# Kernel tuning notes

Hardware: AMD Instinct MI355X
Metric: run time of the kernel (lower is better)

The kernel has to match this reference:

```python
import jax, jax.numpy as jnp
import numpy as np

DMODEL = 1024
Q_HEADS = 16
KV_HEADS = 4
DHEAD = 64
SEQ = 2048
TOP_K = 64
ROPE_BASE = 10000.0
NEG_INF = -1e30  # stand-in for -inf that is safe under softmax


def rope_cos_sin(seq_len, dhead, base):
    inv_freq = 1.0 / (base ** (jnp.arange(0, dhead, 2, dtype=jnp.float32) / dhead))  # [dhead/2]
    t = jnp.arange(seq_len, dtype=jnp.float32)
    angles = jnp.outer(t, inv_freq)                       # [S, dhead/2]
    emb = jnp.concatenate([angles, angles], axis=-1)      # [S, dhead]
    return jnp.cos(emb), jnp.sin(emb)


def rotate_half(x):
    x1, x2 = jnp.split(x, 2, axis=-1)
    return jnp.concatenate([-x2, x1], axis=-1)


def apply_rope(x, cos, sin):
    # x: [B, H, S, dhead]; cos/sin: [S, dhead]
    return x * cos[None, None] + rotate_half(x) * sin[None, None]


def setup_inputs() -> dict:
    key = jax.random.key(0)
    ks = jax.random.split(key, 5)
    s = 0.02
    return {
        "x": jax.random.normal(ks[0], (1, SEQ, DMODEL), jnp.float32),
        "Wq": jax.random.normal(ks[1], (Q_HEADS * DHEAD, DMODEL), jnp.float32) * s,
        "Wk": jax.random.normal(ks[2], (KV_HEADS * DHEAD, DMODEL), jnp.float32) * s,
        "Wv": jax.random.normal(ks[3], (KV_HEADS * DHEAD, DMODEL), jnp.float32) * s,
        "Wo": jax.random.normal(ks[4], (DMODEL, Q_HEADS * DHEAD), jnp.float32) * s,
    }


def reference(x, Wq, Wk, Wv, Wo):
    B, S, _ = x.shape
    cos, sin = rope_cos_sin(S, DHEAD, ROPE_BASE)

    q = (x @ Wq.T).reshape(B, S, Q_HEADS, DHEAD).transpose(0, 2, 1, 3)   # [B,Hq,S,d]
    k = (x @ Wk.T).reshape(B, S, KV_HEADS, DHEAD).transpose(0, 2, 1, 3)  # [B,Hkv,S,d]
    v = (x @ Wv.T).reshape(B, S, KV_HEADS, DHEAD).transpose(0, 2, 1, 3)

    q = apply_rope(q, cos, sin)
    k = apply_rope(k, cos, sin)

    groups = Q_HEADS // KV_HEADS  # repeat_kv
    k = jnp.repeat(k, groups, axis=1)  # [B,Hq,S,d]
    v = jnp.repeat(v, groups, axis=1)

    scores = jnp.einsum("bhqd,bhkd->bhqk", q, k) / np.sqrt(DHEAD)  # [B,H,S,S]

    causal_mask = jnp.triu(jnp.ones((S, S), bool), k=1)
    scores = jnp.where(causal_mask[None, None], NEG_INF, scores)

    # top-k mask before softmax
    topk_vals, _ = jax.lax.top_k(scores, TOP_K)            # [B,H,S,K]
    threshold = topk_vals[..., -1:]                         # kth largest
    scores = jnp.where(scores < threshold, NEG_INF, scores)

    weights = jax.nn.softmax(scores, axis=-1)
    out = jnp.einsum("bhqk,bhkd->bhqd", weights, v)         # [B,H,S,d]
    out = out.transpose(0, 2, 1, 3).reshape(B, S, Q_HEADS * DHEAD)
    return out @ Wo.T
```

## Files before the change

### kernel.cpp

```cpp
#include <hip/hip_runtime.h>
#include <hip/hip_bf16.h>
#include <math.h>

#define SEQ 2048
#define DMODEL 1024
#define QH 16
#define KVH 4
#define DH 64
#define TOPK 64
#define KV_D (KVH * DH)
#define CCAP 512
#define SROW 1028

typedef __attribute__((ext_vector_type(8))) short short8;
typedef __attribute__((ext_vector_type(4))) float floatx4;

__device__ __forceinline__ unsigned f2u(float f) {
    unsigned u = __float_as_uint(f);
    return (u & 0x80000000u) ? ~u : (u | 0x80000000u);
}
__device__ __forceinline__ float u2f(unsigned u) {
    unsigned v = (u & 0x80000000u) ? (u & 0x7fffffffu) : ~u;
    return __uint_as_float(v);
}
__device__ __forceinline__ unsigned short f2bf(float x) {
    unsigned u = __float_as_uint(x);
    return (unsigned short)((u + 0x7fffu + ((u >> 16) & 1u)) >> 16);
}
__device__ __forceinline__ float bf2f(unsigned short h) {
    return __uint_as_float((unsigned)h << 16);
}
__device__ __forceinline__ void split4(float4 f, ushort4& h, ushort4& l) {
    h.x = f2bf(f.x); l.x = f2bf(f.x - bf2f(h.x));
    h.y = f2bf(f.y); l.y = f2bf(f.y - bf2f(h.y));
    h.z = f2bf(f.z); l.z = f2bf(f.z - bf2f(h.z));
    h.w = f2bf(f.w); l.w = f2bf(f.w - bf2f(h.w));
}

__global__ __launch_bounds__(256) void cvt_all(const float* __restrict__ x,
                                               const float* __restrict__ Wq,
                                               const float* __restrict__ Wk,
                                               const float* __restrict__ Wv,
                                               const float* __restrict__ Wo,
                                               unsigned short* __restrict__ xhi,
                                               unsigned short* __restrict__ xlo,
                                               unsigned short* __restrict__ wbhi,
                                               unsigned short* __restrict__ wblo,
                                               unsigned short* __restrict__ wo,
                                               float* __restrict__ cosT,
                                               float* __restrict__ sinT) {
    int idx = blockIdx.x * 256 + threadIdx.x;
    if (idx >= 1196032) return;
    float4 f;
    ushort4 h, l;
    if (idx < 524288) {
        f = ((const float4*)x)[idx];
        split4(f, h, l);
        ((ushort4*)xhi)[idx] = h;
        ((ushort4*)xlo)[idx] = l;
    } else if (idx < 786432) {
        int s = idx - 524288;
        f = ((const float4*)Wq)[s];
        split4(f, h, l);
        ((ushort4*)wbhi)[s] = h;
        ((ushort4*)wblo)[s] = l;
    } else if (idx < 851968) {
        int s = idx - 786432;
        f = ((const float4*)Wk)[s];
        split4(f, h, l);
        ((ushort4*)wbhi)[idx - 524288] = h;
        ((ushort4*)wblo)[idx - 524288] = l;
    } else if (idx < 917504) {
        int s = idx - 851968;
        f = ((const float4*)Wv)[s];
        split4(f, h, l);
        ((ushort4*)wbhi)[idx - 524288] = h;
        ((ushort4*)wblo)[idx - 524288] = l;
    } else if (idx < 1179648) {
        int s = idx - 917504;
        f = ((const float4*)Wo)[s];
        ushort4 o;
        o.x = f2bf(f.x); o.y = f2bf(f.y); o.z = f2bf(f.z); o.w = f2bf(f.w);
        ((ushort4*)wo)[s] = o;
    } else {
        int s = idx - 1179648;
        int e0 = s * 4;
        float ft = (float)(e0 >> 5);
        int d0 = e0 & 31;
        float4 cw, sw;
#pragma unroll
        for (int k = 0; k < 4; ++k) {
            float inv = powf(10000.0f, -(float)(d0 + k) * (1.0f / 32.0f));
            float ss, cc;
            sincosf(ft * inv, &ss, &cc);
            ((float*)&cw)[k] = cc;
            ((float*)&sw)[k] = ss;
        }
        ((float4*)cosT)[s] = cw;
        ((float4*)sinT)[s] = sw;
    }
}

__device__ __forceinline__ void async16(const void* g, void* l) {
    __builtin_amdgcn_global_load_lds(
        (const __attribute__((address_space(1))) unsigned int*)g,
        (__attribute__((address_space(3))) unsigned int*)l, 16, 0, 0);
}

__global__ __launch_bounds__(256, 2) void gemm_qkv(const unsigned short* __restrict__ Ah,
                                                   const unsigned short* __restrict__ Al,
                                                   const unsigned short* __restrict__ Bh,
                                                   const unsigned short* __restrict__ Bl,
                                                   const float* __restrict__ cosT,
                                                   const float* __restrict__ sinT,
                                                   unsigned short* __restrict__ qhi,
                                                   unsigned short* __restrict__ qlo,
                                                   unsigned short* __restrict__ khi,
                                                   unsigned short* __restrict__ klo,
                                                   float* __restrict__ vv) {
    const int K = DMODEL;
    __shared__ unsigned short lAh[128 * 32];
    __shared__ unsigned short lAl[128 * 32];
    __shared__ unsigned short lBh[128 * 32];
    __shared__ unsigned short lBl[128 * 32];
    const int tid = threadIdx.x;
    const int lane = tid & 63;
    const int wid = tid >> 6;
    const int m0 = blockIdx.y * 128, n0 = blockIdx.x * 128;
    const int mq = (wid >> 1) * 64, nq = (wid & 1) * 64;
    const bool isv = (n0 >= 1280);

    floatx4 acc[4][4];
#pragma unroll
    for (int a = 0; a < 4; ++a)
#pragma unroll
        for (int b = 0; b < 4; ++b) acc[a][b] = (floatx4){0.f, 0.f, 0.f, 0.f};

    const int srow = tid >> 2;
    const int skb = (tid & 3) ^ ((tid >> 3) & 3);
    const size_t goff = (size_t)srow * K + skb * 8;
    const size_t goff2 = goff + (size_t)64 * K;
    const unsigned short* pAh = Ah + (size_t)m0 * K;
    const unsigned short* pAl = Al + (size_t)m0 * K;
    const unsigned short* pBh = Bh + (size_t)n0 * K;
    const unsigned short* pBl = Bl + (size_t)n0 * K;
    unsigned lbase = __builtin_amdgcn_readfirstlane((unsigned)(wid * 1024));

    for (int k0 = 0; k0 < K; k0 += 32) {
        async16(pAh + goff + k0, (char*)lAh + lbase);
        async16(pAh + goff2 + k0, (char*)lAh + lbase + 4096);
        async16(pBh + goff + k0, (char*)lBh + lbase);
        async16(pBh + goff2 + k0, (char*)lBh + lbase + 4096);
        if (!isv) {
            async16(pAl + goff + k0, (char*)lAl + lbase);
            async16(pAl + goff2 + k0, (char*)lAl + lbase + 4096);
            async16(pBl + goff + k0, (char*)lBl + lbase);
            async16(pBl + goff2 + k0, (char*)lBl + lbase + 4096);
        }
        __syncthreads();

        short8 ah[4], al[4], bh[4], bl[4];
#pragma unroll
        for (int mt = 0; mt < 4; ++mt) {
            int row = mq + mt * 16 + (lane & 15);
            int s = ((lane >> 4) ^ ((row >> 1) & 3)) * 8;
            ah[mt] = *(const short8*)&lAh[row * 32 + s];
            if (!isv) al[mt] = *(const short8*)&lAl[row * 32 + s];
        }
#pragma unroll
        for (int nt = 0; nt < 4; ++nt) {
            int row = nq + nt * 16 + (lane & 15);
            int s = ((lane >> 4) ^ ((row >> 1) & 3)) * 8;
            bh[nt] = *(const short8*)&lBh[row * 32 + s];
            if (!isv) bl[nt] = *(const short8*)&lBl[row * 32 + s];
        }
        if (isv) {
#pragma unroll
            for (int mt = 0; mt < 4; ++mt)
#pragma unroll
                for (int nt = 0; nt < 4; ++nt)
                    acc[mt][nt] = __builtin_amdgcn_mfma_f32_16x16x32_bf16(ah[mt], bh[nt], acc[mt][nt], 0, 0, 0);
        } else {
#pragma unroll
            for (int mt = 0; mt < 4; ++mt)
#pragma unroll
                for (int nt = 0; nt < 4; ++nt) {
                    floatx4 a = acc[mt][nt];
                    a = __builtin_amdgcn_mfma_f32_16x16x32_bf16(al[mt], bh[nt], a, 0, 0, 0);
                    a = __builtin_amdgcn_mfma_f32_16x16x32_bf16(ah[mt], bl[nt], a, 0, 0, 0);
                    a = __builtin_amdgcn_mfma_f32_16x16x32_bf16(ah[mt], bh[nt], a, 0, 0, 0);
                    acc[mt][nt] = a;
                }
        }
        __syncthreads();
    }

    if (!isv) {
        const bool isq = (n0 < 1024);
        const float qsc = isq ? 0.125f : 1.0f;
#pragma unroll
        for (int mt = 0; mt < 4; ++mt)
#pragma unroll
            for (int nt = 0; nt < 2; ++nt) {
                const int d32 = nt * 16 + (lane & 15);
#pragma unroll
                for (int rr = 0; rr < 4; ++rr) {
                    int row = m0 + mq + mt * 16 + (lane >> 4) * 4 + rr;
                    float lo = acc[mt][nt][rr], hi = acc[mt][nt + 2][rr];
                    float c = cosT[row * 32 + d32], s = sinT[row * 32 + d32];
                    float rlo = (lo * c - hi * s) * qsc;
                    float rhi = (hi * c + lo * s) * qsc;
                    unsigned short hlo = f2bf(rlo), hhi = f2bf(rhi);
                    unsigned short llo = f2bf(rlo - bf2f(hlo));
                    unsigned short lhi = f2bf(rhi - bf2f(hhi));
                    if (isq) {
                        size_t o = (size_t)row * DMODEL + n0 + nq + d32;
                        qhi[o] = hlo; qhi[o + 32] = hhi;
                        qlo[o] = llo; qlo[o + 32] = lhi;
                    } else {
                        int kvh = (n0 + nq - 1024) >> 6;
                        size_t o = ((size_t)kvh * SEQ + row) * DH + d32;
                        khi[o] = hlo; khi[o + 32] = hhi;
                        klo[o] = llo; klo[o + 32] = lhi;
                    }
                }
            }
    } else {
#pragma unroll
        for (int mt = 0; mt < 4; ++mt)
#pragma unroll
            for (int nt = 0; nt < 4; ++nt) {
                int vcol = n0 + nq + nt * 16 + (lane & 15) - 1280;
                int rbase = m0 + mq + mt * 16 + (lane >> 4) * 4;
#pragma unroll
                for (int rr = 0; rr < 4; ++rr)
                    vv[(size_t)(rbase + rr) * KV_D + vcol] = acc[mt][nt][rr];
            }
    }
}

__global__ __launch_bounds__(256, 2) void gemm_wo(const unsigned short* __restrict__ A,
                                                  const unsigned short* __restrict__ B,
                                                  float* __restrict__ C) {
    const int N = DMODEL, K = DMODEL;
    __shared__ unsigned short lAs[64 * 32];
    __shared__ unsigned short lBs[128 * 32];
    const int tid = threadIdx.x;
    const int lane = tid & 63;
    const int wid = tid >> 6;
    const int m0 = blockIdx.y * 64, n0 = blockIdx.x * 128;

    floatx4 acc[4][2];
#pragma unroll
    for (int a = 0; a < 4; ++a)
#pragma unroll
        for (int b = 0; b < 2; ++b) acc[a][b] = (floatx4){0.f, 0.f, 0.f, 0.f};

    const int srow = tid >> 2;
    const int skb = (tid & 3) ^ ((tid >> 3) & 3);
    const unsigned short* Ag = A + (size_t)(m0 + srow) * K + skb * 8;
    const unsigned short* Bg = B + (size_t)(n0 + srow) * K + skb * 8;
    unsigned lbase = __builtin_amdgcn_readfirstlane((unsigned)(wid * 1024));

    for (int k0 = 0; k0 < K; k0 += 32) {
        async16(Ag + k0, (char*)lAs + lbase);
        async16(Bg + k0, (char*)lBs + lbase);
        async16(Bg + (size_t)64 * K + k0, (char*)lBs + lbase + 4096);
        __syncthreads();

        short8 af[4], bf[2];
#pragma unroll
        for (int mt = 0; mt < 4; ++mt) {
            int row = mt * 16 + (lane & 15);
            int s = ((lane >> 4) ^ ((row >> 1) & 3)) * 8;
            af[mt] = *(const short8*)&lAs[row * 32 + s];
        }
#pragma unroll
        for (int nt = 0; nt < 2; ++nt) {
            int row = wid * 32 + nt * 16 + (lane & 15);
            int s = ((lane >> 4) ^ ((row >> 1) & 3)) * 8;
            bf[nt] = *(const short8*)&lBs[row * 32 + s];
        }
#pragma unroll
        for (int mt = 0; mt < 4; ++mt)
#pragma unroll
            for (int nt = 0; nt < 2; ++nt)
                acc[mt][nt] = __builtin_amdgcn_mfma_f32_16x16x32_bf16(af[mt], bf[nt], acc[mt][nt], 0, 0, 0);
        __syncthreads();
    }
#pragma unroll
    for (int mt = 0; mt < 4; ++mt)
#pragma unroll
        for (int nt = 0; nt < 2; ++nt) {
            int col = n0 + wid * 32 + nt * 16 + (lane & 15);
            int rbase = m0 + mt * 16 + (lane >> 4) * 4;
#pragma unroll
            for (int rr = 0; rr < 4; ++rr)
                C[(size_t)(rbase + rr) * N + col] = acc[mt][nt][rr];
        }
}

__device__ __forceinline__ void av_group(float w, int jbase, const float* __restrict__ vb,
                                         float& acc) {
    unsigned long long mk = __ballot(w > 0.f);
    while (mk) {
        int l = __ffsll((unsigned long long)mk) - 1;
        mk &= mk - 1;
        float wj = __shfl(w, l, 64);
        acc += wj * vb[(size_t)(jbase + l * 4) * KV_D];
    }
}

__device__ __forceinline__ void score_chunk(const unsigned short* __restrict__ khi,
                                            const unsigned short* __restrict__ klo,
                                            float* __restrict__ S,
                                            const short8& ah0, const short8& ah1,
                                            const short8& al0, const short8& al1,
                                            int kvh, int w, int lane, int imax, int cbase) {
    const int koff = (lane >> 4) * 8;
#pragma unroll
    for (int n = 0; n < 4; ++n) {
        int jbi = cbase + w + n * 16;
        int jb = jbi * 16;
        if (jb <= imax) {
            size_t bidx = ((size_t)kvh * SEQ + jb + (lane & 15)) * DH + koff;
            short8 bh0 = *(const short8*)(khi + bidx);
            short8 bh1 = *(const short8*)(khi + bidx + 32);
            short8 bl0 = *(const short8*)(klo + bidx);
            short8 bl1 = *(const short8*)(klo + bidx + 32);
            floatx4 acc = (floatx4){0.f, 0.f, 0.f, 0.f};
            acc = __builtin_amdgcn_mfma_f32_16x16x32_bf16(al0, bh0, acc, 0, 0, 0);
            acc = __builtin_amdgcn_mfma_f32_16x16x32_bf16(al1, bh1, acc, 0, 0, 0);
            acc = __builtin_amdgcn_mfma_f32_16x16x32_bf16(ah0, bl0, acc, 0, 0, 0);
            acc = __builtin_amdgcn_mfma_f32_16x16x32_bf16(ah1, bl1, acc, 0, 0, 0);
            acc = __builtin_amdgcn_mfma_f32_16x16x32_bf16(ah0, bh0, acc, 0, 0, 0);
            acc = __builtin_amdgcn_mfma_f32_16x16x32_bf16(ah1, bh1, acc, 0, 0, 0);
            int col = (jb & 1023) + (lane & 15);
            int rbase = (lane >> 4) * 4;
#pragma unroll
            for (int rr = 0; rr < 4; ++rr)
                S[(size_t)(rbase + rr) * SROW + col] = acc[rr];
        }
    }
}

__global__ __launch_bounds__(1024, 8) void attn_block(const unsigned short* __restrict__ qhi,
                                                      const unsigned short* __restrict__ qlo,
                                                      const unsigned short* __restrict__ khi,
                                                      const unsigned short* __restrict__ klo,
                                                      const float* __restrict__ v,
                                                      unsigned short* __restrict__ outb) {
    extern __shared__ float S[];
    const int lane = threadIdx.x & 63;
    const int w = threadIdx.x >> 6;
    const int t = 127 - blockIdx.x;
    const int h = blockIdx.y;
    const int kvh = h >> 2;
    const int m0 = t * 16;
    const int imax = m0 + 15;

    const int arow = m0 + (lane & 15);
    const int koff = (lane >> 4) * 8;
    size_t aidx = (size_t)arow * DMODEL + h * DH + koff;
    short8 ah0 = *(const short8*)(qhi + aidx);
    short8 ah1 = *(const short8*)(qhi + aidx + 32);
    short8 al0 = *(const short8*)(qlo + aidx);
    short8 al1 = *(const short8*)(qlo + aidx + 32);

    const int irow = m0 + w;
    const int cmax = (irow >> 8) + 1;
    float* Srow = S + (size_t)w * SROW;
    uint4 uv[8];
#pragma unroll
    for (int c = 0; c < 8; ++c) uv[c] = make_uint4(0u, 0u, 0u, 0u);

    score_chunk(khi, klo, S, ah0, ah1, al0, al1, kvh, w, lane, imax, 0);
    __syncthreads();
#pragma unroll
    for (int c = 0; c < 4; ++c) {
        if (c < cmax) {
            const int j0 = c * 256 + lane * 4;
            float4 f = *(const float4*)&Srow[j0];
            uv[c].x = (j0 + 0 <= irow) ? f2u(f.x) : 0u;
            uv[c].y = (j0 + 1 <= irow) ? f2u(f.y) : 0u;
            uv[c].z = (j0 + 2 <= irow) ? f2u(f.z) : 0u;
            uv[c].w = (j0 + 3 <= irow) ? f2u(f.w) : 0u;
        }
    }
    __syncthreads();

    if (imax >= 1024) {
        score_chunk(khi, klo, S, ah0, ah1, al0, al1, kvh, w, lane, imax, 64);
    }
    __syncthreads();
#pragma unroll
    for (int c = 4; c < 8; ++c) {
        if (c < cmax) {
            const int j0 = (c - 4) * 256 + lane * 4;
            float4 f = *(const float4*)&Srow[j0];
            int jg = c * 256 + lane * 4;
            uv[c].x = (jg + 0 <= irow) ? f2u(f.x) : 0u;
            uv[c].y = (jg + 1 <= irow) ? f2u(f.y) : 0u;
            uv[c].z = (jg + 2 <= irow) ? f2u(f.z) : 0u;
            uv[c].w = (jg + 3 <= irow) ? f2u(f.w) : 0u;
        }
    }
    __syncthreads();

    unsigned lmax = 0u;
#pragma unroll
    for (int c = 0; c < 8; ++c)
        lmax = max(lmax, max(max(uv[c].x, uv[c].y), max(uv[c].z, uv[c].w)));
    unsigned um = lmax, Lb = lmax;
#pragma unroll
    for (int o = 32; o > 0; o >>= 1) {
        um = max(um, (unsigned)__shfl_xor((int)um, o, 64));
        Lb = min(Lb, (unsigned)__shfl_xor((int)Lb, o, 64));
    }
    const float mf = u2f(um);
    const unsigned long long lmask = (lane == 0) ? 0ull : (~0ull >> (64 - lane));

    uint2* cand = (uint2*)Srow;
    const unsigned thr0 = Lb ? Lb : 1u;
    int nc = 0;
#pragma unroll
    for (int c = 0; c < 8; ++c) {
        if (c < cmax) {
#pragma unroll
            for (int e = 0; e < 4; ++e) {
                unsigned u = (e == 0) ? uv[c].x : (e == 1) ? uv[c].y : (e == 2) ? uv[c].z : uv[c].w;
                bool kp = (u >= thr0);
                unsigned long long mk = __ballot(kp);
                if (kp) {
                    int pos = nc + __popcll(mk & lmask);
                    if (pos < CCAP)
                        cand[pos] = make_uint2(u, (unsigned)(c * 256 + lane * 4 + e));
                }
                nc += (int)__popcll(mk);
            }
        }
    }

    const float* vb = v + kvh * DH + lane;
    float acc = 0.f, den = 0.f;

    if (nc <= CCAP) {
        unsigned cu[8];
#pragma unroll
        for (int tt = 0; tt < 8; ++tt) {
            int idx = tt * 64 + lane;
            unsigned uu = cand[idx].x;
            cu[tt] = (idx < nc) ? uu : 0u;
        }

        unsigned p = 1u;
        if (irow >= TOPK) {
            unsigned diff = Lb ^ um;
            if (diff == 0u) {
                p = um;
            } else {
                int hb = 31 - __builtin_clz(diff);
                p = (hb >= 31) ? 0u : ((um >> (hb + 1)) << (hb + 1));
                for (int b = hb; b >= 0; --b) {
                    unsigned cv = p | (1u << b);
                    int cnt = 0;
#pragma unroll
                    for (int tt = 0; tt < 8; ++tt)
                        cnt += __popcll(__ballot(cu[tt] >= cv));
                    if (cnt >= TOPK) p = cv;
                }
            }
        }

        int kc = 0;
#pragma unroll
        for (int tt = 0; tt < 8; ++tt) {
            int idx = tt * 64 + lane;
            uint2 e = cand[idx];
            bool kp = (idx < nc) && (e.x >= p);
            unsigned long long mk = __ballot(kp);
            if (kp) {
                int pos = kc + __popcll(mk & lmask);
                ((float2*)cand)[pos] = make_float2(__expf(u2f(e.x) - mf),
                                                   __uint_as_float(e.y));
            }
            kc += (int)__popcll(mk);
        }

        float2* pl = (float2*)cand;
        int l = 0;
        for (; l + 16 <= kc; l += 16) {
            float2 pr[16];
            float vx[16];
#pragma unroll
            for (int u = 0; u < 16; ++u) pr[u] = pl[l + u];
#pragma unroll
            for (int u = 0; u < 16; ++u)
                vx[u] = vb[(size_t)__float_as_int(pr[u].y) * KV_D];
#pragma unroll
            for (int u = 0; u < 16; ++u) { den += pr[u].x; acc += pr[u].x * vx[u]; }
        }
        for (; l < kc; ++l) {
            float2 pp = pl[l];
            den += pp.x;
            acc += pp.x * vb[(size_t)__float_as_int(pp.y) * KV_D];
        }
    } else {
        unsigned p = 1u;
        if (irow >= TOPK) {
            unsigned diff = Lb ^ um;
            if (diff == 0u) {
                p = um;
            } else {
                int hb = 31 - __builtin_clz(diff);
                p = (hb >= 31) ? 0u : ((um >> (hb + 1)) << (hb + 1));
                for (int b = hb; b >= 0; --b) {
                    unsigned cv = p | (1u << b);
                    int cnt = 0;
#pragma unroll
                    for (int c = 0; c < 8; ++c) {
                        if (c < cmax) {
                            cnt += __popcll(__ballot(uv[c].x >= cv));
                            cnt += __popcll(__ballot(uv[c].y >= cv));
                            cnt += __popcll(__ballot(uv[c].z >= cv));
                            cnt += __popcll(__ballot(uv[c].w >= cv));
                        }
                    }
                    if (cnt >= TOPK) p = cv;
                }
            }
        }

        float2* pl = (float2*)Srow;
        int base = 0;
#pragma unroll
        for (int c = 0; c < 8; ++c) {
            if (c < cmax) {
#pragma unroll
                for (int e = 0; e < 4; ++e) {
                    unsigned u = (e == 0) ? uv[c].x : (e == 1) ? uv[c].y : (e == 2) ? uv[c].z : uv[c].w;
                    bool kp = (u >= p);
                    unsigned long long mk = __ballot(kp);
                    if (kp) {
                        int pos = base + __popcll(mk & lmask);
                        if (pos < CCAP)
                            pl[pos] = make_float2(__expf(u2f(u) - mf),
                                                  __int_as_float(c * 256 + lane * 4 + e));
                    }
                    base += (int)__popcll(mk);
                }
            }
        }

        if (base <= CCAP) {
            for (int l = 0; l < base; ++l) {
                float2 pp = pl[l];
                den += pp.x;
                acc += pp.x * vb[(size_t)__float_as_int(pp.y) * KV_D];
            }
        } else {
            float lsum = 0.f;
#pragma unroll
            for (int c = 0; c < 8; ++c) {
                if (c < cmax) {
                    float w0 = (uv[c].x >= p) ? __expf(u2f(uv[c].x) - mf) : 0.f;
                    float w1 = (uv[c].y >= p) ? __expf(u2f(uv[c].y) - mf) : 0.f;
                    float w2 = (uv[c].z >= p) ? __expf(u2f(uv[c].z) - mf) : 0.f;
                    float w3 = (uv[c].w >= p) ? __expf(u2f(uv[c].w) - mf) : 0.f;
                    lsum += (w0 + w1) + (w2 + w3);
                    av_group(w0, c * 256 + 0, vb, acc);
                    av_group(w1, c * 256 + 1, vb, acc);
                    av_group(w2, c * 256 + 2, vb, acc);
                    av_group(w3, c * 256 + 3, vb, acc);
                }
            }
            den = lsum;
#pragma unroll
            for (int o = 32; o > 0; o >>= 1) den += __shfl_xor(den, o, 64);
        }
    }

    outb[(size_t)irow * DMODEL + h * DH + lane] = f2bf(acc / den);
}

extern "C" void kernel_launch(void* const* d_in, const int* in_sizes, int n_in,
                              void* d_out, int out_size, void* d_ws, size_t ws_size,
                              hipStream_t stream) {
    const float* x  = (const float*)d_in[0];
    const float* Wq = (const float*)d_in[1];
    const float* Wk = (const float*)d_in[2];
    const float* Wv = (const float*)d_in[3];
    const float* Wo = (const float*)d_in[4];
    float* out = (float*)d_out;

    float* ws = (float*)d_ws;
    float* vv   = ws;
    float* cosT = vv + (size_t)SEQ * KV_D;
    float* sinT = cosT + SEQ * 32;
    unsigned short* bfp = (unsigned short*)(sinT + SEQ * 32);
    unsigned short* xhi  = bfp;  bfp += (size_t)SEQ * DMODEL;
    unsigned short* xlo  = bfp;  bfp += (size_t)SEQ * DMODEL;
    unsigned short* wbhi = bfp;  bfp += (size_t)1536 * DMODEL;
    unsigned short* wblo = bfp;  bfp += (size_t)1536 * DMODEL;
    unsigned short* wob  = bfp;  bfp += (size_t)DMODEL * DMODEL;
    unsigned short* qhi  = bfp;  bfp += (size_t)SEQ * DMODEL;
    unsigned short* qlo  = bfp;  bfp += (size_t)SEQ * DMODEL;
    unsigned short* khi  = bfp;  bfp += (size_t)KVH * SEQ * DH;
    unsigned short* klo  = bfp;  bfp += (size_t)KVH * SEQ * DH;
    unsigned short* attnb = xhi;

    dim3 blk(256);

    cvt_all<<<(1196032 + 255) / 256, blk, 0, stream>>>(x, Wq, Wk, Wv, Wo,
                                                       xhi, xlo, wbhi, wblo, wob,
                                                       cosT, sinT);

    gemm_qkv<<<dim3(1536 / 128, SEQ / 128), blk, 0, stream>>>(xhi, xlo, wbhi, wblo,
                                                              cosT, sinT,
                                                              qhi, qlo, khi, klo, vv);

    const int attn_lds = 16 * SROW * 4;
    hipFuncSetAttribute((const void*)attn_block,
                        hipFuncAttributeMaxDynamicSharedMemorySize, attn_lds);
    attn_block<<<dim3(SEQ / 16, QH), dim3(1024), attn_lds, stream>>>(qhi, qlo, khi, klo, vv, attnb);

    gemm_wo<<<dim3(DMODEL / 128, SEQ / 64), blk, 0, stream>>>(attnb, wob, out);
}
```

Before: 318.4 us.

## Shrink QKV GEMM M-tile to 64 and simplify attention top-k selection path

The QKV GEMM now uses 64-row M tiles, so twice as many blocks are launched and each wave holds fewer accumulators, which should help occupancy and fill more of the GPU. In the attention kernel, the threshold bit-search now runs directly on the register-held scores instead of first compacting up to 512 candidates into LDS. Survivors are compacted once with a 128-entry cap, and the dense fallback handles overflow. One __syncthreads before the selection is also dropped; this relies on each wave only touching its own LDS row.

```diff
diff --git a/kernel.cpp b/kernel.cpp
--- a/kernel.cpp
+++ b/kernel.cpp
@@ -9,7 +9,7 @@
 #define DH 64
 #define TOPK 64
 #define KV_D (KVH * DH)
-#define CCAP 512
+#define CAP 128
 #define SROW 1028
 
 typedef __attribute__((ext_vector_type(8))) short short8;
@@ -119,70 +119,67 @@
                                                    unsigned short* __restrict__ klo,
                                                    float* __restrict__ vv) {
     const int K = DMODEL;
-    __shared__ unsigned short lAh[128 * 32];
-    __shared__ unsigned short lAl[128 * 32];
+    __shared__ unsigned short lAh[64 * 32];
+    __shared__ unsigned short lAl[64 * 32];
     __shared__ unsigned short lBh[128 * 32];
     __shared__ unsigned short lBl[128 * 32];
     const int tid = threadIdx.x;
     const int lane = tid & 63;
     const int wid = tid >> 6;
-    const int m0 = blockIdx.y * 128, n0 = blockIdx.x * 128;
-    const int mq = (wid >> 1) * 64, nq = (wid & 1) * 64;
+    const int m0 = blockIdx.y * 64, n0 = blockIdx.x * 128;
+    const int mh = (wid >> 1) * 32;
+    const int nh = (wid & 1) * 64;
     const bool isv = (n0 >= 1280);
 
-    floatx4 acc[4][4];
-#pragma unroll
-    for (int a = 0; a < 4; ++a)
+    floatx4 acc[2][4];
+#pragma unroll
+    for (int a = 0; a < 2; ++a)
 #pragma unroll
         for (int b = 0; b < 4; ++b) acc[a][b] = (floatx4){0.f, 0.f, 0.f, 0.f};
 
     const int srow = tid >> 2;
     const int skb = (tid & 3) ^ ((tid >> 3) & 3);
-    const size_t goff = (size_t)srow * K + skb * 8;
-    const size_t goff2 = goff + (size_t)64 * K;
-    const unsigned short* pAh = Ah + (size_t)m0 * K;
-    const unsigned short* pAl = Al + (size_t)m0 * K;
-    const unsigned short* pBh = Bh + (size_t)n0 * K;
-    const unsigned short* pBl = Bl + (size_t)n0 * K;
+    const unsigned short* pAh = Ah + (size_t)(m0 + srow) * K + skb * 8;
+    const unsigned short* pAl = Al + (size_t)(m0 + srow) * K + skb * 8;
+    const unsigned short* pBh = Bh + (size_t)(n0 + srow) * K + skb * 8;
+    const unsigned short* pBl = Bl + (size_t)(n0 + srow) * K + skb * 8;
     unsigned lbase = __builtin_amdgcn_readfirstlane((unsigned)(wid * 1024));
 
     for (int k0 = 0; k0 < K; k0 += 32) {
-        async16(pAh + goff + k0, (char*)lAh + lbase);
-        async16(pAh + goff2 + k0, (char*)lAh + lbase + 4096);
-        async16(pBh + goff + k0, (char*)lBh + lbase);
-        async16(pBh + goff2 + k0, (char*)lBh + lbase + 4096);
+        async16(pAh + k0, (char*)lAh + lbase);
+        async16(pBh + k0, (char*)lBh + lbase);
+        async16(pBh + (size_t)64 * K + k0, (char*)lBh + lbase + 4096);
         if (!isv) {
-            async16(pAl + goff + k0, (char*)lAl + lbase);
-            async16(pAl + goff2 + k0, (char*)lAl + lbase + 4096);
-            async16(pBl + goff + k0, (char*)lBl + lbase);
-            async16(pBl + goff2 + k0, (char*)lBl + lbase + 4096);
+            async16(pAl + k0, (char*)lAl + lbase);
+            async16(pBl + k0, (char*)lBl + lbase);
+            async16(pBl + (size_t)64 * K + k0, (char*)lBl + lbase + 4096);
         }
         __syncthreads();
 
-        short8 ah[4], al[4], bh[4], bl[4];
-#pragma unroll
-        for (int mt = 0; mt < 4; ++mt) {
-            int row = mq + mt * 16 + (lane & 15);
+        short8 ah[2], al[2], bh[4], bl[4];
+#pragma unroll
+        for (int mt = 0; mt < 2; ++mt) {
+            int row = mh + mt * 16 + (lane & 15);
             int s = ((lane >> 4) ^ ((row >> 1) & 3)) * 8;
             ah[mt] = *(const short8*)&lAh[row * 32 + s];
             if (!isv) al[mt] = *(const short8*)&lAl[row * 32 + s];
         }
 #pragma unroll
         for (int nt = 0; nt < 4; ++nt) {
-            int row = nq + nt * 16 + (lane & 15);
+            int row = nh + nt * 16 + (lane & 15);
             int s = ((lane >> 4) ^ ((row >> 1) & 3)) * 8;
             bh[nt] = *(const short8*)&lBh[row * 32 + s];
             if (!isv) bl[nt] = *(const short8*)&lBl[row * 32 + s];
         }
         if (isv) {
 #pragma unroll
-            for (int mt = 0; mt < 4; ++mt)
+            for (int mt = 0; mt < 2; ++mt)
 #pragma unroll
                 for (int nt = 0; nt < 4; ++nt)
                     acc[mt][nt] = __builtin_amdgcn_mfma_f32_16x16x32_bf16(ah[mt], bh[nt], acc[mt][nt], 0, 0, 0);
         } else {
 #pragma unroll
-            for (int mt = 0; mt < 4; ++mt)
+            for (int mt = 0; mt < 2; ++mt)
 #pragma unroll
                 for (int nt = 0; nt < 4; ++nt) {
                     floatx4 a = acc[mt][nt];
@@ -195,17 +192,18 @@
         __syncthreads();
     }
 
+    const int cb = n0 + nh;
     if (!isv) {
-        const bool isq = (n0 < 1024);
+        const bool isq = (cb < 1024);
         const float qsc = isq ? 0.125f : 1.0f;
 #pragma unroll
-        for (int mt = 0; mt < 4; ++mt)
+        for (int mt = 0; mt < 2; ++mt)
 #pragma unroll
             for (int nt = 0; nt < 2; ++nt) {
                 const int d32 = nt * 16 + (lane & 15);
 #pragma unroll
                 for (int rr = 0; rr < 4; ++rr) {
-                    int row = m0 + mq + mt * 16 + (lane >> 4) * 4 + rr;
+                    int row = m0 + mh + mt * 16 + (lane >> 4) * 4 + rr;
                     float lo = acc[mt][nt][rr], hi = acc[mt][nt + 2][rr];
                     float c = cosT[row * 32 + d32], s = sinT[row * 32 + d32];
                     float rlo = (lo * c - hi * s) * qsc;
@@ -214,11 +212,11 @@
                     unsigned short llo = f2bf(rlo - bf2f(hlo));
                     unsigned short lhi = f2bf(rhi - bf2f(hhi));
                     if (isq) {
-                        size_t o = (size_t)row * DMODEL + n0 + nq + d32;
+                        size_t o = (size_t)row * DMODEL + cb + d32;
                         qhi[o] = hlo; qhi[o + 32] = hhi;
                         qlo[o] = llo; qlo[o + 32] = lhi;
                     } else {
-                        int kvh = (n0 + nq - 1024) >> 6;
+                        int kvh = (cb - 1024) >> 6;
                         size_t o = ((size_t)kvh * SEQ + row) * DH + d32;
                         khi[o] = hlo; khi[o + 32] = hhi;
                         klo[o] = llo; klo[o + 32] = lhi;
@@ -227,11 +225,11 @@
             }
     } else {
 #pragma unroll
-        for (int mt = 0; mt < 4; ++mt)
+        for (int mt = 0; mt < 2; ++mt)
 #pragma unroll
             for (int nt = 0; nt < 4; ++nt) {
-                int vcol = n0 + nq + nt * 16 + (lane & 15) - 1280;
-                int rbase = m0 + mq + mt * 16 + (lane >> 4) * 4;
+                int vcol = cb + nt * 16 + (lane & 15) - 1280;
+                int rbase = m0 + mh + mt * 16 + (lane >> 4) * 4;
 #pragma unroll
                 for (int rr = 0; rr < 4; ++rr)
                     vv[(size_t)(rbase + rr) * KV_D + vcol] = acc[mt][nt][rr];
@@ -405,7 +403,6 @@
             uv[c].w = (jg + 3 <= irow) ? f2u(f.w) : 0u;
         }
     }
-    __syncthreads();
 
     unsigned lmax = 0u;
 #pragma unroll
@@ -418,78 +415,59 @@
         Lb = min(Lb, (unsigned)__shfl_xor((int)Lb, o, 64));
     }
     const float mf = u2f(um);
+
+    unsigned p = 1u;
+    if (irow >= TOPK) {
+        unsigned diff = Lb ^ um;
+        if (diff == 0u) {
+            p = um;
+        } else {
+            int hb = 31 - __builtin_clz(diff);
+            p = (hb >= 31) ? 0u : ((um >> (hb + 1)) << (hb + 1));
+            for (int b = hb; b >= 0; --b) {
+                unsigned cand = p | (1u << b);
+                int cnt = 0;
+#pragma unroll
+                for (int c = 0; c < 8; ++c) {
+                    if (c < cmax) {
+                        cnt += __popcll(__ballot(uv[c].x >= cand));
+                        cnt += __popcll(__ballot(uv[c].y >= cand));
+                        cnt += __popcll(__ballot(uv[c].z >= cand));
+                        cnt += __popcll(__ballot(uv[c].w >= cand));
+                    }
+                }
+                if (cnt >= TOPK) p = cand;
+            }
+        }
+    }
+
+    float2* pl = (float2*)Srow;
     const unsigned long long lmask = (lane == 0) ? 0ull : (~0ull >> (64 - lane));
-
-    uint2* cand = (uint2*)Srow;
-    const unsigned thr0 = Lb ? Lb : 1u;
-    int nc = 0;
+    int base = 0;
 #pragma unroll
     for (int c = 0; c < 8; ++c) {
         if (c < cmax) {
 #pragma unroll
             for (int e = 0; e < 4; ++e) {
                 unsigned u = (e == 0) ? uv[c].x : (e == 1) ? uv[c].y : (e == 2) ? uv[c].z : uv[c].w;
-                bool kp = (u >= thr0);
+                bool kp = (u >= p);
                 unsigned long long mk = __ballot(kp);
                 if (kp) {
-                    int pos = nc + __popcll(mk & lmask);
-                    if (pos < CCAP)
-                        cand[pos] = make_uint2(u, (unsigned)(c * 256 + lane * 4 + e));
+                    int pos = base + __popcll(mk & lmask);
+                    if (pos < CAP)
+                        pl[pos] = make_float2(__expf(u2f(u) - mf),
+                                              __int_as_float(c * 256 + lane * 4 + e));
                 }
-                nc += (int)__popcll(mk);
+                base += (int)__popcll(mk);
             }
         }
     }
 
     const float* vb = v + kvh * DH + lane;
     float acc = 0.f, den = 0.f;
-
-    if (nc <= CCAP) {
-        unsigned cu[8];
-#pragma unroll
-        for (int tt = 0; tt < 8; ++tt) {
-            int idx = tt * 64 + lane;
-            unsigned uu = cand[idx].x;
-            cu[tt] = (idx < nc) ? uu : 0u;
-        }
-
-        unsigned p = 1u;
-        if (irow >= TOPK) {
-            unsigned diff = Lb ^ um;
-            if (diff == 0u) {
-                p = um;
-            } else {
-                int hb = 31 - __builtin_clz(diff);
-                p = (hb >= 31) ? 0u : ((um >> (hb + 1)) << (hb + 1));
-                for (int b = hb; b >= 0; --b) {
-                    unsigned cv = p | (1u << b);
-                    int cnt = 0;
-#pragma unroll
-                    for (int tt = 0; tt < 8; ++tt)
-                        cnt += __popcll(__ballot(cu[tt] >= cv));
-                    if (cnt >= TOPK) p = cv;
-                }
-            }
-        }
-
-        int kc = 0;
-#pragma unroll
-        for (int tt = 0; tt < 8; ++tt) {
-            int idx = tt * 64 + lane;
-            uint2 e = cand[idx];
-            bool kp = (idx < nc) && (e.x >= p);
-            unsigned long long mk = __ballot(kp);
-            if (kp) {
-                int pos = kc + __popcll(mk & lmask);
-                ((float2*)cand)[pos] = make_float2(__expf(u2f(e.x) - mf),
-                                                   __uint_as_float(e.y));
-            }
-            kc += (int)__popcll(mk);
-        }
-
-        float2* pl = (float2*)cand;
+    if (base <= CAP) {
         int l = 0;
-        for (; l + 16 <= kc; l += 16) {
+        for (; l + 16 <= base; l += 16) {
             float2 pr[16];
             float vx[16];
 #pragma unroll
@@ -500,84 +478,30 @@
 #pragma unroll
             for (int u = 0; u < 16; ++u) { den += pr[u].x; acc += pr[u].x * vx[u]; }
         }
-        for (; l < kc; ++l) {
+        for (; l < base; ++l) {
             float2 pp = pl[l];
             den += pp.x;
             acc += pp.x * vb[(size_t)__float_as_int(pp.y) * KV_D];
         }
     } else {
-        unsigned p = 1u;
-        if (irow >= TOPK) {
-            unsigned diff = Lb ^ um;
-            if (diff == 0u) {
-                p = um;
-            } else {
-                int hb = 31 - __builtin_clz(diff);
-                p = (hb >= 31) ? 0u : ((um >> (hb + 1)) << (hb + 1));
-                for (int b = hb; b >= 0; --b) {
-                    unsigned cv = p | (1u << b);
-                    int cnt = 0;
-#pragma unroll
-                    for (int c = 0; c < 8; ++c) {
-                        if (c < cmax) {
-                            cnt += __popcll(__ballot(uv[c].x >= cv));
-                            cnt += __popcll(__ballot(uv[c].y >= cv));
-                            cnt += __popcll(__ballot(uv[c].z >= cv));
-                            cnt += __popcll(__ballot(uv[c].w >= cv));
-                        }
-                    }
-                    if (cnt >= TOPK) p = cv;
-                }
-            }
-        }
-
-        float2* pl = (float2*)Srow;
-        int base = 0;
+        float lsum = 0.f;
 #pragma unroll
         for (int c = 0; c < 8; ++c) {
             if (c < cmax) {
-#pragma unroll
-                for (int e = 0; e < 4; ++e) {
-                    unsigned u = (e == 0) ? uv[c].x : (e == 1) ? uv[c].y : (e == 2) ? uv[c].z : uv[c].w;
-                    bool kp = (u >= p);
-                    unsigned long long mk = __ballot(kp);
-                    if (kp) {
-                        int pos = base + __popcll(mk & lmask);
-                        if (pos < CCAP)
-                            pl[pos] = make_float2(__expf(u2f(u) - mf),
-                                                  __int_as_float(c * 256 + lane * 4 + e));
-                    }
-                    base += (int)__popcll(mk);
-                }
+                float w0 = (uv[c].x >= p) ? __expf(u2f(uv[c].x) - mf) : 0.f;
+                float w1 = (uv[c].y >= p) ? __expf(u2f(uv[c].y) - mf) : 0.f;
+                float w2 = (uv[c].z >= p) ? __expf(u2f(uv[c].z) - mf) : 0.f;
+                float w3 = (uv[c].w >= p) ? __expf(u2f(uv[c].w) - mf) : 0.f;
+                lsum += (w0 + w1) + (w2 + w3);
+                av_group(w0, c * 256 + 0, vb, acc);
+                av_group(w1, c * 256 + 1, vb, acc);
+                av_group(w2, c * 256 + 2, vb, acc);
+                av_group(w3, c * 256 + 3, vb, acc);
             }
         }
-
-        if (base <= CCAP) {
-            for (int l = 0; l < base; ++l) {
-                float2 pp = pl[l];
-                den += pp.x;
-                acc += pp.x * vb[(size_t)__float_as_int(pp.y) * KV_D];
-            }
-        } else {
-            float lsum = 0.f;
-#pragma unroll
-            for (int c = 0; c < 8; ++c) {
-                if (c < cmax) {
-                    float w0 = (uv[c].x >= p) ? __expf(u2f(uv[c].x) - mf) : 0.f;
-                    float w1 = (uv[c].y >= p) ? __expf(u2f(uv[c].y) - mf) : 0.f;
-                    float w2 = (uv[c].z >= p) ? __expf(u2f(uv[c].z) - mf) : 0.f;
-                    float w3 = (uv[c].w >= p) ? __expf(u2f(uv[c].w) - mf) : 0.f;
-                    lsum += (w0 + w1) + (w2 + w3);
-                    av_group(w0, c * 256 + 0, vb, acc);
-                    av_group(w1, c * 256 + 1, vb, acc);
-                    av_group(w2, c * 256 + 2, vb, acc);
-                    av_group(w3, c * 256 + 3, vb, acc);
-                }
-            }
-            den = lsum;
-#pragma unroll
-            for (int o = 32; o > 0; o >>= 1) den += __shfl_xor(den, o, 64);
-        }
+        den = lsum;
+#pragma unroll
+        for (int o = 32; o > 0; o >>= 1) den += __shfl_xor(den, o, 64);
     }
 
     outb[(size_t)irow * DMODEL + h * DH + lane] = f2bf(acc / den);
@@ -615,9 +539,9 @@
                                                        xhi, xlo, wbhi, wblo, wob,
                                                        cosT, sinT);
 
-    gemm_qkv<<<dim3(1536 / 128, SEQ / 128), blk, 0, stream>>>(xhi, xlo, wbhi, wblo,
-                                                              cosT, sinT,
-                                                              qhi, qlo, khi, klo, vv);
+    gemm_qkv<<<dim3(1536 / 128, SEQ / 64), blk, 0, stream>>>(xhi, xlo, wbhi, wblo,
+                                                             cosT, sinT,
+                                                             qhi, qlo, khi, klo, vv);
 
     const int attn_lds = 16 * SROW * 4;
     hipFuncSetAttribute((const void*)attn_block,
```

Result: faster. 302.4 us (-5.0%).
